# Kernel tuning notes

Measured on AMD Instinct MI355X. Metric: run time of the kernel, lower is better.

Reference implementation:

```python
import jax, jax.numpy as jnp
import numpy as np

ALPHA = 0.2  # LeakyReLU slope


def _gat_scores(Wh, a_src, a_dst):
    # Wh: (..., N, H); score[i, j] = a_src . Wh_i + a_dst . Wh_j
    s_src = jnp.einsum('...nh,...h->...n', Wh, a_src)
    s_dst = jnp.einsum('...nh,...h->...n', Wh, a_dst)
    e = jax.nn.leaky_relu(s_src[..., :, None] + s_dst[..., None, :], ALPHA)
    # adj is all-ones -> mask is a no-op; softmax over neighbors j
    return jax.nn.softmax(e, axis=-1)


def setup_inputs() -> dict:
    key = jax.random.key(0)
    ks = jax.random.split(key, 9)
    B, S, F = 32, 12, 128
    H, K, C, N = 64, 8, 64, 512

    def xavier(k, shape, gain=1.414):
        fan_in, fan_out = shape[-2], shape[-1]
        lim = gain * np.sqrt(6.0 / (fan_in + fan_out))
        return jax.random.uniform(k, shape, jnp.float32, -lim, lim)

    x = jax.random.normal(ks[0], (B, S, F), jnp.float32)
    W_heads = xavier(ks[1], (K, F, H))
    a_heads = xavier(ks[2], (K, 2 * H, 1))[..., 0]  # (K, 2H)
    a1_heads, a2_heads = a_heads[:, :H], a_heads[:, H:]
    W_out = xavier(ks[3], (K * H, C))
    a_out = xavier(ks[4], (2 * C, 1))[:, 0]
    a1_out, a2_out = a_out[:C], a_out[C:]
    lim = 1.0 / np.sqrt(N * C)
    Wf = jax.random.uniform(ks[5], (C, N * C), jnp.float32, -lim, lim)
    bf = jax.random.uniform(ks[6], (C,), jnp.float32, -lim, lim)
    return {"x": x, "W_heads": W_heads, "a1_heads": a1_heads,
            "a2_heads": a2_heads, "W_out": W_out, "a1_out": a1_out,
            "a2_out": a2_out, "Wf": Wf, "bf": bf}


def reference(x, W_heads, a1_heads, a2_heads, W_out, a1_out, a2_out, Wf, bf):
    N = 512
    B = x.shape[0]
    h = jnp.broadcast_to(x[:, -1, None, :], (B, N, x.shape[-1]))  # (B, N, F)

    # Multi-head GAT, heads vectorized: Wh (B, K, N, H)
    Wh = jnp.einsum('bnf,kfh->bknh', h, W_heads)
    att = _gat_scores(Wh, a1_heads, a2_heads)            # (B, K, N, N)
    hp = jnp.einsum('bkij,bkjh->bkih', att, Wh)           # (B, K, N, H)
    hp = jax.nn.elu(hp)
    B_, K, N_, H = hp.shape
    h_cat = hp.transpose(0, 2, 1, 3).reshape(B_, N_, K * H)  # concat heads

    # Output GAT layer (concat=False -> no ELU)
    Wh_o = jnp.einsum('bnf,fc->bnc', h_cat, W_out)        # (B, N, C)
    att_o = _gat_scores(Wh_o, a1_out, a2_out)             # (B, N, N)
    out = jnp.einsum('bij,bjc->bic', att_o, Wh_o)         # (B, N, C)

    out = out.reshape(B, -1)
    return out @ Wf.T + bf
```

## Files before the change

kernel.cpp:

```cpp
#include <hip/hip_runtime.h>
#include <hip/hip_bf16.h>


__global__ __launch_bounds__(256) void k_wfsum(const float* __restrict__ Wf,
                                               float* __restrict__ wsum) {
    const int bx    = blockIdx.x;
    const int c     = bx >> 2;
    const int chunk = bx & 3;
    const int t = threadIdx.x;
    const int p = t & 15;
    const int g = t >> 4;
    const float* row = Wf + (size_t)c * 32768;

    float acc[4] = {0.f, 0.f, 0.f, 0.f};
#pragma unroll
    for (int i = 0; i < 8; ++i) {
        const int n = chunk * 128 + g + 16 * i;
        const float4 v = *reinterpret_cast<const float4*>(row + n * 64 + p * 4);
        acc[0] += v.x; acc[1] += v.y; acc[2] += v.z; acc[3] += v.w;
    }
    __shared__ float s[16][64];
#pragma unroll
    for (int e = 0; e < 4; ++e) s[g][p * 4 + e] = acc[e];
    __syncthreads();
    if (t < 64) {
        float sum = 0.f;
#pragma unroll
        for (int g2 = 0; g2 < 16; ++g2) sum += s[g2][t];
        wsum[chunk * 4096 + t * 64 + c] = sum;
    }
}

__global__ __launch_bounds__(256) void k_main(const float* __restrict__ x,
                                              const float* __restrict__ W_heads,
                                              const float* __restrict__ W_out,
                                              const float* __restrict__ bias,
                                              const float* __restrict__ wsum,
                                              float* __restrict__ out) {
    const int b = blockIdx.x;
    const int t = threadIdx.x;

    __shared__ float xl[128];
    __shared__ float hp[512];
    __shared__ float who[64];
    __shared__ float red[256];

    if (t < 128) xl[t] = x[b * 1536 + 11 * 128 + t];
    __syncthreads();

    {
        const int k = t >> 5;
        const int h = (t & 31) * 2;
        const float* wb = W_heads + k * 8192 + h;
        float a0 = 0.f, a1 = 0.f;
#pragma unroll 8
        for (int f = 0; f < 128; ++f) {
            const float2 v = *reinterpret_cast<const float2*>(wb + f * 64);
            const float xv = xl[f];
            a0 += xv * v.x;
            a1 += xv * v.y;
        }
        hp[k * 64 + h]     = (a0 > 0.f) ? a0 : expm1f(a0);
        hp[k * 64 + h + 1] = (a1 > 0.f) ? a1 : expm1f(a1);
    }
    __syncthreads();

    {
        const int c  = t & 63;
        const int jg = t >> 6;
        float acc = 0.f;
#pragma unroll 8
        for (int j = jg * 128; j < jg * 128 + 128; ++j)
            acc += hp[j] * W_out[j * 64 + c];
        red[t] = acc;
    }
    __syncthreads();
    if (t < 64) who[t] = red[t] + red[t + 64] + red[t + 128] + red[t + 192];
    __syncthreads();

    {
        const int c  = t & 63;
        const int cg = t >> 6;
        float acc = 0.f;
#pragma unroll
        for (int c2 = cg * 16; c2 < cg * 16 + 16; ++c2) {
            const int o = c2 * 64 + c;
            const float w = wsum[o] + wsum[4096 + o] + wsum[8192 + o] + wsum[12288 + o];
            acc += who[c2] * w;
        }
        red[t] = acc;
    }
    __syncthreads();
    if (t < 64)
        out[b * 64 + t] = red[t] + red[t + 64] + red[t + 128] + red[t + 192] + bias[t];
}

extern "C" void kernel_launch(void* const* d_in, const int* in_sizes, int n_in,
                              void* d_out, int out_size, void* d_ws, size_t ws_size,
                              hipStream_t stream) {
    const float* x       = (const float*)d_in[0];
    const float* W_heads = (const float*)d_in[1];
    const float* W_out   = (const float*)d_in[4];
    const float* Wf      = (const float*)d_in[7];
    const float* bias    = (const float*)d_in[8];
    float* wsum = (float*)d_ws;

    k_wfsum<<<256, 256, 0, stream>>>(Wf, wsum);
    k_main<<<32, 256, 0, stream>>>(x, W_heads, W_out, bias, wsum, (float*)d_out);
}
```

Measured before the change: 88.05 us.

## Move head projection into parallel first kernel alongside Wf reduction

Splits the per-head projection across 128 blocks that run in the same launch as the Wf column-sum, and writes the ELU outputs to workspace. The second kernel then only does the W_out and final projections using vectorized loads. The aim is to remove the serial, low-occupancy head projection from the 32-block main kernel. In exchange, the Wf reduction now uses 64 blocks instead of 256, so each block reads more data.

```diff
diff --git a/kernel.cpp b/kernel.cpp
--- a/kernel.cpp
+++ b/kernel.cpp
@@ -2,80 +2,104 @@
 #include <hip/hip_bf16.h>
 
 
-__global__ __launch_bounds__(256) void k_wfsum(const float* __restrict__ Wf,
-                                               float* __restrict__ wsum) {
-    const int bx    = blockIdx.x;
-    const int c     = bx >> 2;
-    const int chunk = bx & 3;
+__global__ __launch_bounds__(256) void kA(const float* __restrict__ Wf,
+                                          const float* __restrict__ x,
+                                          const float* __restrict__ W_heads,
+                                          float* __restrict__ ws) {
+    float* wsumT = ws;
+    float* HP    = ws + 4096;
     const int t = threadIdx.x;
-    const int p = t & 15;
-    const int g = t >> 4;
-    const float* row = Wf + (size_t)c * 32768;
 
-    float acc[4] = {0.f, 0.f, 0.f, 0.f};
+    if (blockIdx.x < 64) {
+        const int c = blockIdx.x;
+        const float* row = Wf + (size_t)c * 32768;
+        const int p = t & 15;
+        const int ng = t >> 4;
+        float ax = 0.f, ay = 0.f, az = 0.f, aw = 0.f;
+#pragma unroll 8
+        for (int i = 0; i < 32; ++i) {
+            const float4 v = *reinterpret_cast<const float4*>(row + (ng + 16 * i) * 64 + p * 4);
+            ax += v.x; ay += v.y; az += v.z; aw += v.w;
+        }
+        __shared__ float s[16][64];
+        s[ng][p * 4 + 0] = ax; s[ng][p * 4 + 1] = ay;
+        s[ng][p * 4 + 2] = az; s[ng][p * 4 + 3] = aw;
+        __syncthreads();
+        if (t < 64) {
+            float sum = 0.f;
 #pragma unroll
-    for (int i = 0; i < 8; ++i) {
-        const int n = chunk * 128 + g + 16 * i;
-        const float4 v = *reinterpret_cast<const float4*>(row + n * 64 + p * 4);
-        acc[0] += v.x; acc[1] += v.y; acc[2] += v.z; acc[3] += v.w;
+            for (int g = 0; g < 16; ++g) sum += s[g][t];
+            wsumT[t * 64 + c] = sum;
+        }
+    } else {
+        const int idx = blockIdx.x - 64;
+        const int k  = idx >> 4;
+        const int hq = (idx & 15) * 4;
+        __shared__ float xl[32][129];
+#pragma unroll
+        for (int r = 0; r < 4; ++r) {
+            const int id = t + 256 * r;
+            const int b = id >> 5, fq = id & 31;
+            const float4 v = *reinterpret_cast<const float4*>(x + b * 1536 + 1408 + fq * 4);
+            xl[b][fq * 4 + 0] = v.x; xl[b][fq * 4 + 1] = v.y;
+            xl[b][fq * 4 + 2] = v.z; xl[b][fq * 4 + 3] = v.w;
+        }
+        __syncthreads();
+        const int fh = t & 1;
+        const int e  = (t >> 1) & 3;
+        const int b  = t >> 3;
+        const float* wp = W_heads + k * 8192 + fh * 4096 + hq + e;
+        float acc = 0.f;
+#pragma unroll 16
+        for (int f = 0; f < 64; ++f)
+            acc += xl[b][fh * 64 + f] * wp[f * 64];
+        acc += __shfl_xor(acc, 1);
+        if (fh == 0) {
+            const float v = (acc > 0.f) ? acc : expm1f(acc);
+            HP[b * 512 + k * 64 + hq + e] = v;
+        }
     }
+}
+
+__global__ __launch_bounds__(256) void kB(const float* __restrict__ W_out,
+                                          const float* __restrict__ bias,
+                                          const float* __restrict__ ws,
+                                          float* __restrict__ out) {
+    const float* wsumT = ws;
+    const float* HP    = ws + 4096;
+    const int b = blockIdx.x;
+    const int t = threadIdx.x;
+
+    __shared__ float hp[512];
     __shared__ float s[16][64];
-#pragma unroll
-    for (int e = 0; e < 4; ++e) s[g][p * 4 + e] = acc[e];
+    __shared__ float who[64];
+    __shared__ float red[256];
+
+    hp[t]       = HP[b * 512 + t];
+    hp[t + 256] = HP[b * 512 + 256 + t];
+    __syncthreads();
+
+    {
+        const int cq = t & 15;
+        const int jg = t >> 4;
+        float ax = 0.f, ay = 0.f, az = 0.f, aw = 0.f;
+#pragma unroll 8
+        for (int i = 0; i < 32; ++i) {
+            const int j = jg + 16 * i;
+            const float4 w = *reinterpret_cast<const float4*>(W_out + j * 64 + cq * 4);
+            const float h = hp[j];
+            ax += h * w.x; ay += h * w.y; az += h * w.z; aw += h * w.w;
+        }
+        s[jg][cq * 4 + 0] = ax; s[jg][cq * 4 + 1] = ay;
+        s[jg][cq * 4 + 2] = az; s[jg][cq * 4 + 3] = aw;
+    }
     __syncthreads();
     if (t < 64) {
         float sum = 0.f;
 #pragma unroll
-        for (int g2 = 0; g2 < 16; ++g2) sum += s[g2][t];
-        wsum[chunk * 4096 + t * 64 + c] = sum;
+        for (int g = 0; g < 16; ++g) sum += s[g][t];
+        who[t] = sum;
     }
-}
-
-__global__ __launch_bounds__(256) void k_main(const float* __restrict__ x,
-                                              const float* __restrict__ W_heads,
-                                              const float* __restrict__ W_out,
-                                              const float* __restrict__ bias,
-                                              const float* __restrict__ wsum,
-                                              float* __restrict__ out) {
-    const int b = blockIdx.x;
-    const int t = threadIdx.x;
-
-    __shared__ float xl[128];
-    __shared__ float hp[512];
-    __shared__ float who[64];
-    __shared__ float red[256];
-
-    if (t < 128) xl[t] = x[b * 1536 + 11 * 128 + t];
-    __syncthreads();
-
-    {
-        const int k = t >> 5;
-        const int h = (t & 31) * 2;
-        const float* wb = W_heads + k * 8192 + h;
-        float a0 = 0.f, a1 = 0.f;
-#pragma unroll 8
-        for (int f = 0; f < 128; ++f) {
-            const float2 v = *reinterpret_cast<const float2*>(wb + f * 64);
-            const float xv = xl[f];
-            a0 += xv * v.x;
-            a1 += xv * v.y;
-        }
-        hp[k * 64 + h]     = (a0 > 0.f) ? a0 : expm1f(a0);
-        hp[k * 64 + h + 1] = (a1 > 0.f) ? a1 : expm1f(a1);
-    }
-    __syncthreads();
-
-    {
-        const int c  = t & 63;
-        const int jg = t >> 6;
-        float acc = 0.f;
-#pragma unroll 8
-        for (int j = jg * 128; j < jg * 128 + 128; ++j)
-            acc += hp[j] * W_out[j * 64 + c];
-        red[t] = acc;
-    }
-    __syncthreads();
-    if (t < 64) who[t] = red[t] + red[t + 64] + red[t + 128] + red[t + 192];
     __syncthreads();
 
     {
@@ -83,11 +107,8 @@
         const int cg = t >> 6;
         float acc = 0.f;
 #pragma unroll
-        for (int c2 = cg * 16; c2 < cg * 16 + 16; ++c2) {
-            const int o = c2 * 64 + c;
-            const float w = wsum[o] + wsum[4096 + o] + wsum[8192 + o] + wsum[12288 + o];
-            acc += who[c2] * w;
-        }
+        for (int c2 = cg * 16; c2 < cg * 16 + 16; ++c2)
+            acc += who[c2] * wsumT[c2 * 64 + c];
         red[t] = acc;
     }
     __syncthreads();
@@ -103,8 +124,8 @@
     const float* W_out   = (const float*)d_in[4];
     const float* Wf      = (const float*)d_in[7];
     const float* bias    = (const float*)d_in[8];
-    float* wsum = (float*)d_ws;
+    float* ws = (float*)d_ws;
 
-    k_wfsum<<<256, 256, 0, stream>>>(Wf, wsum);
-    k_main<<<32, 256, 0, stream>>>(x, W_heads, W_out, bias, wsum, (float*)d_out);
+    kA<<<192, 256, 0, stream>>>(Wf, x, W_heads, ws);
+    kB<<<32, 256, 0, stream>>>(W_out, bias, ws, (float*)d_out);
 }
```

Measured after the change: 80.58 us. 1.09x faster.
